# Performance work log

Measured on AMD Instinct MI355X. Metric: run time of the kernel, lower is better.

Reference implementation:

```python
import jax, jax.numpy as jnp
import numpy as np

B, T, D = 1, 4096, 1024
H = 16
HEAD_DIM = D // H
WINDOW = 256


def setup_inputs() -> dict:
    key = jax.random.key(0)
    k1, k2, k3 = jax.random.split(key, 3)
    x = jax.random.normal(k1, (B, T, D), dtype=jnp.float32)
    # torch nn.Linear(D, 3D) weight is (3D, D); we store transposed (D, 3D) for x @ W
    w_qkv = jax.random.normal(k2, (D, 3 * D), dtype=jnp.float32) * (1.0 / np.sqrt(D))
    w_out = jax.random.normal(k3, (D, D), dtype=jnp.float32) * (1.0 / np.sqrt(D))
    return {"x": x, "w_qkv": w_qkv, "w_out": w_out}


def reference(x, w_qkv, w_out):
    b, t, d = x.shape
    qkv = x @ w_qkv                                   # (B, T, 3D)
    q, k, v = jnp.split(qkv, 3, axis=-1)
    def split_heads(a):                               # (B, T, D) -> (B, H, T, dh)
        return a.reshape(b, t, H, HEAD_DIM).transpose(0, 2, 1, 3)
    q, k, v = split_heads(q), split_heads(k), split_heads(v)
    scale = jnp.sqrt(jnp.float32(HEAD_DIM))
    scores = jnp.einsum('bhqd,bhkd->bhqk', q, k) / scale   # (B, H, T, T)
    rows = jnp.arange(t)[:, None]
    cols = jnp.arange(t)[None, :]
    # causal sliding window: j <= i and j >= i - window + 1
    mask = (cols <= rows) & (cols >= rows - WINDOW + 1)     # (T, T) bool
    scores = jnp.where(mask[None, None], scores, -jnp.inf)
    attn = jax.nn.softmax(scores, axis=-1)
    out = jnp.einsum('bhqk,bhkd->bhqd', attn, v)            # (B, H, T, dh)
    out = out.transpose(0, 2, 1, 3).reshape(b, t, d)        # merge heads
    return out @ w_out
```

## Files before the change

### kernel.cpp

```cpp
#include <hip/hip_runtime.h>
#include <hip/hip_bf16.h>

#define T_SEQ 4096
#define DMODEL 1024
#define NH 16
#define DH 64
#define N_QKV 3072
#define N_QK 2048

typedef __attribute__((ext_vector_type(8))) short bf16x8;
typedef __attribute__((ext_vector_type(4))) float f32x4;

__device__ inline void gload_lds16(const __hip_bfloat16* g, __hip_bfloat16* l) {
  __builtin_amdgcn_global_load_lds(
      (const __attribute__((address_space(1))) void*)g,
      (__attribute__((address_space(3))) void*)l, 16, 0, 0);
}

__global__ void prep_kernel(const float* __restrict__ x,
                            const float* __restrict__ w_qkv,
                            const float* __restrict__ w_out,
                            __hip_bfloat16* __restrict__ x_bf,
                            __hip_bfloat16* __restrict__ wqkvT,
                            __hip_bfloat16* __restrict__ woutT) {
  __shared__ float tile[32][33];
  const int b = blockIdx.x;
  if (b < 4096) {
    int i = (b * 256 + threadIdx.x) * 4;
    float4 v = *(const float4*)(x + i);
    ushort4 o;
    o.x = __bfloat16_as_ushort(__float2bfloat16(v.x));
    o.y = __bfloat16_as_ushort(__float2bfloat16(v.y));
    o.z = __bfloat16_as_ushort(__float2bfloat16(v.z));
    o.w = __bfloat16_as_ushort(__float2bfloat16(v.w));
    *(ushort4*)((unsigned short*)x_bf + i) = o;
    return;
  }
  const float* in;
  __hip_bfloat16* out;
  int NN, KK, bn, bk;
  if (b < 7168) {
    int idx = b - 4096;
    in = w_qkv; out = wqkvT; NN = N_QKV; KK = DMODEL;
    bn = (idx % 96) * 32; bk = (idx / 96) * 32;
  } else {
    int idx = b - 7168;
    in = w_out; out = woutT; NN = DMODEL; KK = DMODEL;
    bn = (idx % 32) * 32; bk = (idx / 32) * 32;
  }
  int tx = threadIdx.x & 31, ty = threadIdx.x >> 5;
#pragma unroll
  for (int r = 0; r < 32; r += 8)
    tile[ty + r][tx] = in[(size_t)(bk + ty + r) * NN + bn + tx];
  __syncthreads();
#pragma unroll
  for (int r = 0; r < 32; r += 8)
    out[(size_t)(bn + ty + r) * KK + bk + tx] = __float2bfloat16(tile[tx][ty + r]);
}

__global__ __launch_bounds__(512, 2) void gemm8_qkv(
    const __hip_bfloat16* __restrict__ A, const __hip_bfloat16* __restrict__ Bt,
    __hip_bfloat16* __restrict__ qk, __hip_bfloat16* __restrict__ vt) {
  const int K = DMODEL;
  __shared__ alignas(16) __hip_bfloat16 Ab[3][256 * 64];
  __shared__ alignas(16) __hip_bfloat16 Bb[2][192 * 64];

  const int tid = threadIdx.x;
  const int lane = tid & 63;
  const int w = tid >> 6;
  const int wr = w >> 2, wc = w & 3;
  const int frow = lane & 15, fgrp = lane >> 4;

  const int bid = blockIdx.x;
  const int sbid = (bid & 7) * 32 + (bid >> 3);
  const int mb = sbid >> 4, nb = sbid & 15;
  const int brow = mb << 8, bcol = nb * 192;

  const int srow = lane >> 3;
  const int sslot = (lane & 7) ^ srow;
  const __hip_bfloat16* aSrcA = A + (size_t)(brow + w * 32 + srow) * K + sslot * 8;
  const __hip_bfloat16* aSrcB = Bt + (size_t)(bcol + w * 24 + srow) * K + sslot * 8;
  const int dstA = (w * 32 + srow) * 64 + (lane & 7) * 8;
  const int dstB = (w * 24 + srow) * 64 + (lane & 7) * 8;

  f32x4 acc[8][3] = {};

#pragma unroll
  for (int i = 0; i < 4; i++)
    gload_lds16(aSrcA + (size_t)(i * 8) * K, &Ab[0][dstA + i * 8 * 64]);
#pragma unroll
  for (int i = 0; i < 3; i++)
    gload_lds16(aSrcB + (size_t)(i * 8) * K, &Bb[0][dstB + i * 8 * 64]);
#pragma unroll
  for (int i = 0; i < 4; i++)
    gload_lds16(aSrcA + (size_t)(i * 8) * K + 64, &Ab[1][dstA + i * 8 * 64]);

  for (int t = 0; t < 16; ++t) {
    if (t < 15)
      asm volatile("s_waitcnt vmcnt(4)" ::: "memory");
    else
      asm volatile("s_waitcnt vmcnt(0)" ::: "memory");
    __builtin_amdgcn_s_barrier();

    const __hip_bfloat16* As = &Ab[t % 3][0];
    const __hip_bfloat16* Bs = &Bb[t & 1][0];
    bf16x8 bfrag[3][2], afrag[4][2];

#pragma unroll
    for (int n = 0; n < 3; n++) {
      int row = wc * 48 + n * 16 + frow;
#pragma unroll
      for (int kh = 0; kh < 2; kh++) {
        int slot = (kh * 4 + fgrp) ^ (row & 7);
        bfrag[n][kh] = *(const bf16x8*)(Bs + row * 64 + slot * 8);
      }
    }
#pragma unroll
    for (int m = 0; m < 4; m++) {
      int row = wr * 128 + m * 16 + frow;
#pragma unroll
      for (int kh = 0; kh < 2; kh++) {
        int slot = (kh * 4 + fgrp) ^ (row & 7);
        afrag[m][kh] = *(const bf16x8*)(As + row * 64 + slot * 8);
      }
    }
    if (t + 1 < 16) {
      __hip_bfloat16* bd = &Bb[(t + 1) & 1][0];
#pragma unroll
      for (int i = 0; i < 3; i++)
        gload_lds16(aSrcB + (size_t)(i * 8) * K + (t + 1) * 64, bd + dstB + i * 8 * 64);
    }
    __builtin_amdgcn_s_barrier();
    __builtin_amdgcn_s_setprio(1);
#pragma unroll
    for (int m = 0; m < 4; m++)
#pragma unroll
      for (int n = 0; n < 3; n++) {
        acc[m][n] = __builtin_amdgcn_mfma_f32_16x16x32_bf16(afrag[m][0], bfrag[n][0], acc[m][n], 0, 0, 0);
        acc[m][n] = __builtin_amdgcn_mfma_f32_16x16x32_bf16(afrag[m][1], bfrag[n][1], acc[m][n], 0, 0, 0);
      }
    __builtin_amdgcn_s_setprio(0);
    __builtin_amdgcn_s_barrier();

#pragma unroll
    for (int m = 0; m < 4; m++) {
      int row = wr * 128 + (m + 4) * 16 + frow;
#pragma unroll
      for (int kh = 0; kh < 2; kh++) {
        int slot = (kh * 4 + fgrp) ^ (row & 7);
        afrag[m][kh] = *(const bf16x8*)(As + row * 64 + slot * 8);
      }
    }
    if (t + 2 < 16) {
      __hip_bfloat16* ad = &Ab[(t + 2) % 3][0];
#pragma unroll
      for (int i = 0; i < 4; i++)
        gload_lds16(aSrcA + (size_t)(i * 8) * K + (t + 2) * 64, ad + dstA + i * 8 * 64);
    }
    __builtin_amdgcn_s_barrier();
    __builtin_amdgcn_s_setprio(1);
#pragma unroll
    for (int m = 0; m < 4; m++)
#pragma unroll
      for (int n = 0; n < 3; n++) {
        acc[m + 4][n] = __builtin_amdgcn_mfma_f32_16x16x32_bf16(afrag[m][0], bfrag[n][0], acc[m + 4][n], 0, 0, 0);
        acc[m + 4][n] = __builtin_amdgcn_mfma_f32_16x16x32_bf16(afrag[m][1], bfrag[n][1], acc[m + 4][n], 0, 0, 0);
      }
    __builtin_amdgcn_s_setprio(0);
  }

  const int orow0 = brow + wr * 128 + 4 * fgrp;
  const int ocol0 = bcol + wc * 48 + frow;
#pragma unroll
  for (int m = 0; m < 8; m++)
#pragma unroll
    for (int n = 0; n < 3; n++) {
      int col = ocol0 + n * 16;
      int row0 = orow0 + m * 16;
      if (col < N_QK) {
        float sc = (col < DMODEL) ? 0.125f : 1.0f;
#pragma unroll
        for (int j = 0; j < 4; j++)
          qk[(size_t)(row0 + j) * N_QK + col] = __float2bfloat16(acc[m][n][j] * sc);
      } else {
        ushort4 pack;
        pack.x = __bfloat16_as_ushort(__float2bfloat16(acc[m][n][0]));
        pack.y = __bfloat16_as_ushort(__float2bfloat16(acc[m][n][1]));
        pack.z = __bfloat16_as_ushort(__float2bfloat16(acc[m][n][2]));
        pack.w = __bfloat16_as_ushort(__float2bfloat16(acc[m][n][3]));
        *(ushort4*)((unsigned short*)vt + (size_t)(col - N_QK) * T_SEQ + row0) = pack;
      }
    }
}

__global__ __launch_bounds__(256) void gemm_out(
    const __hip_bfloat16* __restrict__ A, const __hip_bfloat16* __restrict__ Bt,
    float* __restrict__ C) {
  const int K = DMODEL, N = DMODEL;
  __shared__ alignas(16) __hip_bfloat16 Ab[4][128 * 32];
  __shared__ alignas(16) __hip_bfloat16 Bb[4][128 * 32];
  const int tid = threadIdx.x, lane = tid & 63, w = tid >> 6;
  const int wr = w >> 1, wc = w & 1;
  const int frow = lane & 15, fgrp = lane >> 4;
  const int bid = blockIdx.x;
  const int sbid = (bid & 7) * 32 + (bid >> 3);
  const int mb = sbid >> 3, nb = sbid & 7;
  const int brow = mb * 128, bcol = nb * 128;

  const int sr = tid >> 2;
  const int swz = ((tid & 3) ^ ((sr >> 1) & 3)) << 3;
  const __hip_bfloat16* aA = A + (size_t)(brow + sr) * K + swz;
  const __hip_bfloat16* aB = Bt + (size_t)(bcol + sr) * K + swz;
  const int dlo = sr * 32 + (tid & 3) * 8;
  const int dhi = (sr + 64) * 32 + (tid & 3) * 8;

  f32x4 acc[4][4] = {};
#pragma unroll
  for (int t = 0; t < 3; t++) {
    gload_lds16(aA + t * 32, &Ab[t][dlo]);
    gload_lds16(aA + 64 * (size_t)K + t * 32, &Ab[t][dhi]);
    gload_lds16(aB + t * 32, &Bb[t][dlo]);
    gload_lds16(aB + 64 * (size_t)K + t * 32, &Bb[t][dhi]);
  }
  for (int t = 0; t < 32; ++t) {
    if (t < 30)
      asm volatile("s_waitcnt vmcnt(8)" ::: "memory");
    else if (t == 30)
      asm volatile("s_waitcnt vmcnt(4)" ::: "memory");
    else
      asm volatile("s_waitcnt vmcnt(0)" ::: "memory");
    __builtin_amdgcn_s_barrier();
    const __hip_bfloat16* As = Ab[t & 3];
    const __hip_bfloat16* Bs = Bb[t & 3];
    if (t + 3 < 32) {
      gload_lds16(aA + (t + 3) * 32, &Ab[(t + 3) & 3][dlo]);
      gload_lds16(aA + 64 * (size_t)K + (t + 3) * 32, &Ab[(t + 3) & 3][dhi]);
      gload_lds16(aB + (t + 3) * 32, &Bb[(t + 3) & 3][dlo]);
      gload_lds16(aB + 64 * (size_t)K + (t + 3) * 32, &Bb[(t + 3) & 3][dhi]);
    }
    bf16x8 af[4], bfr[4];
#pragma unroll
    for (int m = 0; m < 4; m++) {
      int row = wr * 64 + m * 16 + frow;
      af[m] = *(const bf16x8*)(As + row * 32 + ((fgrp ^ ((row >> 1) & 3)) << 3));
    }
#pragma unroll
    for (int n = 0; n < 4; n++) {
      int row = wc * 64 + n * 16 + frow;
      bfr[n] = *(const bf16x8*)(Bs + row * 32 + ((fgrp ^ ((row >> 1) & 3)) << 3));
    }
    __builtin_amdgcn_s_barrier();
    __builtin_amdgcn_s_setprio(1);
#pragma unroll
    for (int m = 0; m < 4; m++)
#pragma unroll
      for (int n = 0; n < 4; n++)
        acc[m][n] = __builtin_amdgcn_mfma_f32_16x16x32_bf16(af[m], bfr[n], acc[m][n], 0, 0, 0);
    __builtin_amdgcn_s_setprio(0);
  }
  const int orow0 = brow + wr * 64 + 4 * fgrp;
  const int ocol0 = bcol + wc * 64 + frow;
#pragma unroll
  for (int m = 0; m < 4; m++)
#pragma unroll
    for (int n = 0; n < 4; n++)
#pragma unroll
      for (int j = 0; j < 4; j++)
        C[(size_t)(orow0 + m * 16 + j) * N + ocol0 + n * 16] = acc[m][n][j];
}

__global__ __launch_bounds__(256) void swa_kernel(
    const __hip_bfloat16* __restrict__ qk, const __hip_bfloat16* __restrict__ vt,
    __hip_bfloat16* __restrict__ attn_out) {
  const int b = blockIdx.x;
  const int s = (b & 7) * 128 + (b >> 3);
  const int h = s >> 6;
  const int qb = s & 63;
  const int tid = threadIdx.x;
  const int lane = tid & 63;
  const int w = tid >> 6;
  const int frow = lane & 15;
  const int fgrp = lane >> 4;
  const int fk = fgrp * 8;

  __shared__ alignas(16) __hip_bfloat16 Ks[2][64 * 64];
  __shared__ alignas(16) __hip_bfloat16 Vs[2][64 * 64];
  __shared__ alignas(16) __hip_bfloat16 Pl[4][16 * 72];

  const int qrow_g = qb * 64 + w * 16 + frow;
  bf16x8 aq[2];
  {
    const __hip_bfloat16* qptr = qk + (size_t)qrow_g * N_QK + h * DH;
    aq[0] = *(const bf16x8*)(qptr + fk);
    aq[1] = *(const bf16x8*)(qptr + 32 + fk);
  }

  f32x4 o[4] = {};
  float l_run[4] = {0.f, 0.f, 0.f, 0.f};

  const int srow = lane >> 3;
  const int ssw = (((lane & 7) ^ srow) << 3);
  const __hip_bfloat16* kbase =
      qk + (size_t)(w * 16 + srow) * N_QK + DMODEL + h * DH + ssw;
  const __hip_bfloat16* vbase =
      vt + (size_t)(h * DH + w * 16 + srow) * T_SEQ + ssw;

  const int kb0 = qb >= 4 ? qb - 4 : 0;

  {
    const __hip_bfloat16* ks = kbase + (size_t)kb0 * 64 * N_QK;
    gload_lds16(ks, &Ks[0][w * 16 * 64]);
    gload_lds16(ks + 8 * (size_t)N_QK, &Ks[0][(w * 16 + 8) * 64]);
    const __hip_bfloat16* vs = vbase + kb0 * 64;
    gload_lds16(vs, &Vs[0][w * 16 * 64]);
    gload_lds16(vs + 8 * (size_t)T_SEQ, &Vs[0][(w * 16 + 8) * 64]);
  }

  for (int kb = kb0; kb <= qb; kb++) {
    const int buf = (kb - kb0) & 1;
    if (kb < qb) {
      const __hip_bfloat16* ks = kbase + (size_t)(kb + 1) * 64 * N_QK;
      gload_lds16(ks, &Ks[buf ^ 1][w * 16 * 64]);
      gload_lds16(ks + 8 * (size_t)N_QK, &Ks[buf ^ 1][(w * 16 + 8) * 64]);
      const __hip_bfloat16* vs = vbase + (kb + 1) * 64;
      gload_lds16(vs, &Vs[buf ^ 1][w * 16 * 64]);
      gload_lds16(vs + 8 * (size_t)T_SEQ, &Vs[buf ^ 1][(w * 16 + 8) * 64]);
      asm volatile("s_waitcnt vmcnt(4)" ::: "memory");
    } else {
      asm volatile("s_waitcnt vmcnt(0)" ::: "memory");
    }
    __builtin_amdgcn_s_barrier();

    f32x4 sc[4];
#pragma unroll
    for (int n = 0; n < 4; n++) sc[n] = (f32x4){0.f, 0.f, 0.f, 0.f};
#pragma unroll
    for (int n = 0; n < 4; n++) {
      int rowk = n * 16 + frow;
      int x = rowk & 7;
      bf16x8 bk0 = *(const bf16x8*)(&Ks[buf][rowk * 64 + ((fgrp ^ x) << 3)]);
      bf16x8 bk1 = *(const bf16x8*)(&Ks[buf][rowk * 64 + (((4 + fgrp) ^ x) << 3)]);
      sc[n] = __builtin_amdgcn_mfma_f32_16x16x32_bf16(aq[0], bk0, sc[n], 0, 0, 0);
      sc[n] = __builtin_amdgcn_mfma_f32_16x16x32_bf16(aq[1], bk1, sc[n], 0, 0, 0);
    }

    const bool edge_hi = (kb == qb);
    const bool edge_lo = (kb == qb - 4);
#pragma unroll
    for (int r = 0; r < 4; r++) {
      const int row_l = w * 16 + 4 * fgrp + r;
      float rs = 0.f;
#pragma unroll
      for (int n = 0; n < 4; n++) {
        int col_l = n * 16 + frow;
        bool valid = (!edge_hi || col_l <= row_l) && (!edge_lo || col_l > row_l);
        float p = valid ? __expf(sc[n][r]) : 0.f;
        sc[n][r] = p;
        rs += p;
      }
      l_run[r] += rs;
    }

    __hip_bfloat16* pw = &Pl[w][0];
#pragma unroll
    for (int n = 0; n < 4; n++)
#pragma unroll
      for (int r = 0; r < 4; r++)
        pw[(4 * fgrp + r) * 72 + n * 16 + frow] = __float2bfloat16(sc[n][r]);

#pragma unroll
    for (int c = 0; c < 2; c++) {
      bf16x8 ap = *(const bf16x8*)(pw + frow * 72 + c * 32 + fk);
#pragma unroll
      for (int nd = 0; nd < 4; nd++) {
        int rowd = nd * 16 + frow;
        int x = rowd & 7;
        bf16x8 bv = *(const bf16x8*)(&Vs[buf][rowd * 64 + (((c * 4 + fgrp) ^ x) << 3)]);
        o[nd] = __builtin_amdgcn_mfma_f32_16x16x32_bf16(ap, bv, o[nd], 0, 0, 0);
      }
    }
    __builtin_amdgcn_s_barrier();
  }

#pragma unroll
  for (int r = 0; r < 4; r++) {
    float l = l_run[r];
    l += __shfl_xor(l, 1);
    l += __shfl_xor(l, 2);
    l += __shfl_xor(l, 4);
    l += __shfl_xor(l, 8);
    l_run[r] = l;
  }
#pragma unroll
  for (int nd = 0; nd < 4; nd++)
#pragma unroll
    for (int r = 0; r < 4; r++) {
      float v = o[nd][r] / l_run[r];
      attn_out[(size_t)(qb * 64 + w * 16 + 4 * fgrp + r) * DMODEL + h * DH + nd * 16 + frow] =
          __float2bfloat16(v);
    }
}

extern "C" void kernel_launch(void* const* d_in, const int* in_sizes, int n_in,
                              void* d_out, int out_size, void* d_ws, size_t ws_size,
                              hipStream_t stream) {
  const float* x = (const float*)d_in[0];
  const float* w_qkv = (const float*)d_in[1];
  const float* w_out = (const float*)d_in[2];
  float* out = (float*)d_out;

  char* ws = (char*)d_ws;
  __hip_bfloat16* x_bf = (__hip_bfloat16*)ws;
  __hip_bfloat16* wqkvT = (__hip_bfloat16*)(ws + 8388608);
  __hip_bfloat16* woutT = (__hip_bfloat16*)(ws + 14680064);
  __hip_bfloat16* qk_bf = (__hip_bfloat16*)(ws + 16777216);
  __hip_bfloat16* vt = (__hip_bfloat16*)(ws + 33554432);
  __hip_bfloat16* attn_bf = (__hip_bfloat16*)(ws + 41943040);

  prep_kernel<<<8192, 256, 0, stream>>>(x, w_qkv, w_out, x_bf, wqkvT, woutT);

  gemm8_qkv<<<(T_SEQ / 256) * (N_QKV / 192), 512, 0, stream>>>(x_bf, wqkvT, qk_bf, vt);

  swa_kernel<<<(T_SEQ / 64) * NH, 256, 0, stream>>>(qk_bf, vt, attn_bf);

  gemm_out<<<256, 256, 0, stream>>>(attn_bf, woutT, out);
}
```

Baseline: 83.35 us.

## Retile QKV GEMM to 128x192 blocks with 4 waves and double-buffered loads

The QKV projection GEMM now uses 128x192 output tiles computed by 256-thread blocks (4 waves, each covering 64x96), instead of 256x192 tiles with 8 waves. The launch grid doubles to 512 blocks. The triple-buffered A staging with split half-step compute is replaced by simple double buffering of both A and B, issued at the top of each iteration. This gives more blocks for occupancy and load balance and simplifies synchronisation, at the cost of less A reuse per block and more global traffic for B. The epilogue also writes Q columns twice (unscaled, then scaled), which adds redundant stores.

New measurement: 84.05 us. About the same (+0.8%).

```diff
diff --git a/kernel.cpp b/kernel.cpp
--- a/kernel.cpp
+++ b/kernel.cpp
@@ -58,130 +58,102 @@
     out[(size_t)(bn + ty + r) * KK + bk + tx] = __float2bfloat16(tile[tx][ty + r]);
 }
 
-__global__ __launch_bounds__(512, 2) void gemm8_qkv(
+__global__ __launch_bounds__(256, 2) void gemm8_qkv(
     const __hip_bfloat16* __restrict__ A, const __hip_bfloat16* __restrict__ Bt,
     __hip_bfloat16* __restrict__ qk, __hip_bfloat16* __restrict__ vt) {
   const int K = DMODEL;
-  __shared__ alignas(16) __hip_bfloat16 Ab[3][256 * 64];
+  __shared__ alignas(16) __hip_bfloat16 Ab[2][128 * 64];
   __shared__ alignas(16) __hip_bfloat16 Bb[2][192 * 64];
 
   const int tid = threadIdx.x;
   const int lane = tid & 63;
   const int w = tid >> 6;
-  const int wr = w >> 2, wc = w & 3;
+  const int wr = w >> 1, wc = w & 1;
   const int frow = lane & 15, fgrp = lane >> 4;
 
   const int bid = blockIdx.x;
-  const int sbid = (bid & 7) * 32 + (bid >> 3);
+  const int sbid = (bid & 7) * 64 + (bid >> 3);
   const int mb = sbid >> 4, nb = sbid & 15;
-  const int brow = mb << 8, bcol = nb * 192;
-
-  const int srow = lane >> 3;
-  const int sslot = (lane & 7) ^ srow;
-  const __hip_bfloat16* aSrcA = A + (size_t)(brow + w * 32 + srow) * K + sslot * 8;
-  const __hip_bfloat16* aSrcB = Bt + (size_t)(bcol + w * 24 + srow) * K + sslot * 8;
-  const int dstA = (w * 32 + srow) * 64 + (lane & 7) * 8;
-  const int dstB = (w * 24 + srow) * 64 + (lane & 7) * 8;
-
-  f32x4 acc[8][3] = {};
-
+  const int brow = mb << 7, bcol = nb * 192;
+
+  const int sslot = (tid & 7) ^ ((tid >> 3) & 7);
+  const __hip_bfloat16* aSrcA = A + (size_t)(brow + (tid >> 3)) * K + sslot * 8;
+  const __hip_bfloat16* aSrcB = Bt + (size_t)(bcol + (tid >> 3)) * K + sslot * 8;
+
+  f32x4 acc[4][6] = {};
+
+#pragma unroll
+  for (int i = 0; i < 6; i++)
+    gload_lds16(aSrcB + (size_t)(i * 32) * K, &Bb[0][(i * 256 + tid) * 8]);
 #pragma unroll
   for (int i = 0; i < 4; i++)
-    gload_lds16(aSrcA + (size_t)(i * 8) * K, &Ab[0][dstA + i * 8 * 64]);
-#pragma unroll
-  for (int i = 0; i < 3; i++)
-    gload_lds16(aSrcB + (size_t)(i * 8) * K, &Bb[0][dstB + i * 8 * 64]);
-#pragma unroll
-  for (int i = 0; i < 4; i++)
-    gload_lds16(aSrcA + (size_t)(i * 8) * K + 64, &Ab[1][dstA + i * 8 * 64]);
+    gload_lds16(aSrcA + (size_t)(i * 32) * K, &Ab[0][(i * 256 + tid) * 8]);
 
   for (int t = 0; t < 16; ++t) {
-    if (t < 15)
-      asm volatile("s_waitcnt vmcnt(4)" ::: "memory");
-    else
+    if (t < 15) {
+      __hip_bfloat16* bd = &Bb[(t + 1) & 1][0];
+      __hip_bfloat16* ad = &Ab[(t + 1) & 1][0];
+#pragma unroll
+      for (int i = 0; i < 6; i++)
+        gload_lds16(aSrcB + (size_t)(i * 32) * K + (t + 1) * 64, bd + (i * 256 + tid) * 8);
+#pragma unroll
+      for (int i = 0; i < 4; i++)
+        gload_lds16(aSrcA + (size_t)(i * 32) * K + (t + 1) * 64, ad + (i * 256 + tid) * 8);
+      asm volatile("s_waitcnt vmcnt(10)" ::: "memory");
+    } else {
       asm volatile("s_waitcnt vmcnt(0)" ::: "memory");
-    __builtin_amdgcn_s_barrier();
-
-    const __hip_bfloat16* As = &Ab[t % 3][0];
+    }
+    __builtin_amdgcn_s_barrier();
+
+    const __hip_bfloat16* As = &Ab[t & 1][0];
     const __hip_bfloat16* Bs = &Bb[t & 1][0];
-    bf16x8 bfrag[3][2], afrag[4][2];
-
-#pragma unroll
-    for (int n = 0; n < 3; n++) {
-      int row = wc * 48 + n * 16 + frow;
-#pragma unroll
-      for (int kh = 0; kh < 2; kh++) {
-        int slot = (kh * 4 + fgrp) ^ (row & 7);
-        bfrag[n][kh] = *(const bf16x8*)(Bs + row * 64 + slot * 8);
-      }
+    bf16x8 afr[4][2], bfr[6][2];
+#pragma unroll
+    for (int n = 0; n < 6; n++) {
+      int row = wc * 96 + n * 16 + frow;
+#pragma unroll
+      for (int kh = 0; kh < 2; kh++)
+        bfr[n][kh] = *(const bf16x8*)(Bs + row * 64 + (((kh * 4 + fgrp) ^ (row & 7)) << 3));
     }
 #pragma unroll
     for (int m = 0; m < 4; m++) {
-      int row = wr * 128 + m * 16 + frow;
-#pragma unroll
-      for (int kh = 0; kh < 2; kh++) {
-        int slot = (kh * 4 + fgrp) ^ (row & 7);
-        afrag[m][kh] = *(const bf16x8*)(As + row * 64 + slot * 8);
-      }
-    }
-    if (t + 1 < 16) {
-      __hip_bfloat16* bd = &Bb[(t + 1) & 1][0];
-#pragma unroll
-      for (int i = 0; i < 3; i++)
-        gload_lds16(aSrcB + (size_t)(i * 8) * K + (t + 1) * 64, bd + dstB + i * 8 * 64);
-    }
-    __builtin_amdgcn_s_barrier();
+      int row = wr * 64 + m * 16 + frow;
+#pragma unroll
+      for (int kh = 0; kh < 2; kh++)
+        afr[m][kh] = *(const bf16x8*)(As + row * 64 + (((kh * 4 + fgrp) ^ (row & 7)) << 3));
+    }
+    asm volatile("s_waitcnt lgkmcnt(0)" ::: "memory");
+    __builtin_amdgcn_s_barrier();
+
     __builtin_amdgcn_s_setprio(1);
 #pragma unroll
     for (int m = 0; m < 4; m++)
 #pragma unroll
-      for (int n = 0; n < 3; n++) {
-        acc[m][n] = __builtin_amdgcn_mfma_f32_16x16x32_bf16(afrag[m][0], bfrag[n][0], acc[m][n], 0, 0, 0);
-        acc[m][n] = __builtin_amdgcn_mfma_f32_16x16x32_bf16(afrag[m][1], bfrag[n][1], acc[m][n], 0, 0, 0);
+      for (int n = 0; n < 6; n++) {
+        acc[m][n] = __builtin_amdgcn_mfma_f32_16x16x32_bf16(afr[m][0], bfr[n][0], acc[m][n], 0, 0, 0);
+        acc[m][n] = __builtin_amdgcn_mfma_f32_16x16x32_bf16(afr[m][1], bfr[n][1], acc[m][n], 0, 0, 0);
       }
     __builtin_amdgcn_s_setprio(0);
-    __builtin_amdgcn_s_barrier();
-
-#pragma unroll
-    for (int m = 0; m < 4; m++) {
-      int row = wr * 128 + (m + 4) * 16 + frow;
-#pragma unroll
-      for (int kh = 0; kh < 2; kh++) {
-        int slot = (kh * 4 + fgrp) ^ (row & 7);
-        afrag[m][kh] = *(const bf16x8*)(As + row * 64 + slot * 8);
-      }
-    }
-    if (t + 2 < 16) {
-      __hip_bfloat16* ad = &Ab[(t + 2) % 3][0];
-#pragma unroll
-      for (int i = 0; i < 4; i++)
-        gload_lds16(aSrcA + (size_t)(i * 8) * K + (t + 2) * 64, ad + dstA + i * 8 * 64);
-    }
-    __builtin_amdgcn_s_barrier();
-    __builtin_amdgcn_s_setprio(1);
-#pragma unroll
-    for (int m = 0; m < 4; m++)
-#pragma unroll
-      for (int n = 0; n < 3; n++) {
-        acc[m + 4][n] = __builtin_amdgcn_mfma_f32_16x16x32_bf16(afrag[m][0], bfrag[n][0], acc[m + 4][n], 0, 0, 0);
-        acc[m + 4][n] = __builtin_amdgcn_mfma_f32_16x16x32_bf16(afrag[m][1], bfrag[n][1], acc[m + 4][n], 0, 0, 0);
-      }
-    __builtin_amdgcn_s_setprio(0);
-  }
-
-  const int orow0 = brow + wr * 128 + 4 * fgrp;
-  const int ocol0 = bcol + wc * 48 + frow;
-#pragma unroll
-  for (int m = 0; m < 8; m++)
-#pragma unroll
-    for (int n = 0; n < 3; n++) {
+  }
+
+  const int orow0 = brow + wr * 64 + 4 * fgrp;
+  const int ocol0 = bcol + wc * 96 + frow;
+#pragma unroll
+  for (int m = 0; m < 4; m++)
+#pragma unroll
+    for (int n = 0; n < 6; n++) {
       int col = ocol0 + n * 16;
       int row0 = orow0 + m * 16;
       if (col < N_QK) {
         float sc = (col < DMODEL) ? 0.125f : 1.0f;
 #pragma unroll
         for (int j = 0; j < 4; j++)
-          qk[(size_t)(row0 + j) * N_QK + col] = __float2bfloat16(acc[m][n][j] * sc);
+          qk[(size_t)(row0 + j) * N_QK + col] = __float2bfloat16(acc[m][n][j]);
+        if (col < DMODEL) {
+#pragma unroll
+          for (int j = 0; j < 4; j++)
+            qk[(size_t)(row0 + j) * N_QK + col] = __float2bfloat16(acc[m][n][j] * sc);
+        }
       } else {
         ushort4 pack;
         pack.x = __bfloat16_as_ushort(__float2bfloat16(acc[m][n][0]));
@@ -419,7 +391,7 @@
 
   prep_kernel<<<8192, 256, 0, stream>>>(x, w_qkv, w_out, x_bf, wqkvT, woutT);
 
-  gemm8_qkv<<<(T_SEQ / 256) * (N_QKV / 192), 512, 0, stream>>>(x_bf, wqkvT, qk_bf, vt);
+  gemm8_qkv<<<(T_SEQ / 128) * (N_QKV / 192), 256, 0, stream>>>(x_bf, wqkvT, qk_bf, vt);
 
   swa_kernel<<<(T_SEQ / 64) * NH, 256, 0, stream>>>(qk_bf, vt, attn_bf);
 
```

## Process 128-query tiles per block in sliding-window attention to reuse K/V loads

Applied to the files above, without the earlier changes.

Each attention block now handles 128 query rows (two 16-row groups per wave) instead of 64, so every K/V tile staged in LDS is reused by twice as many queries. The key range widens to 6 blocks per tile, and masking switches to global row/column comparisons. The grid is halved to 512 blocks. In exchange, each block does some wasted masked work on edge tiles, register pressure rises from doubled accumulators, and the smaller grid gives less parallelism across CUs.

After: 84.52 us. No clear change (+1.4%).

```diff
diff --git a/kernel.cpp b/kernel.cpp
--- a/kernel.cpp
+++ b/kernel.cpp
@@ -273,9 +273,10 @@
     const __hip_bfloat16* __restrict__ qk, const __hip_bfloat16* __restrict__ vt,
     __hip_bfloat16* __restrict__ attn_out) {
   const int b = blockIdx.x;
-  const int s = (b & 7) * 128 + (b >> 3);
-  const int h = s >> 6;
-  const int qb = s & 63;
+  const int s = (b & 7) * 64 + (b >> 3);
+  const int h = s >> 5;
+  const int qt = s & 31;
+  const int qs = qt * 128;
   const int tid = threadIdx.x;
   const int lane = tid & 63;
   const int w = tid >> 6;
@@ -287,118 +288,122 @@
   __shared__ alignas(16) __hip_bfloat16 Vs[2][64 * 64];
   __shared__ alignas(16) __hip_bfloat16 Pl[4][16 * 72];
 
-  const int qrow_g = qb * 64 + w * 16 + frow;
-  bf16x8 aq[2];
-  {
-    const __hip_bfloat16* qptr = qk + (size_t)qrow_g * N_QK + h * DH;
-    aq[0] = *(const bf16x8*)(qptr + fk);
-    aq[1] = *(const bf16x8*)(qptr + 32 + fk);
-  }
-
-  f32x4 o[4] = {};
-  float l_run[4] = {0.f, 0.f, 0.f, 0.f};
-
-  const int srow = lane >> 3;
-  const int ssw = (((lane & 7) ^ srow) << 3);
-  const __hip_bfloat16* kbase =
-      qk + (size_t)(w * 16 + srow) * N_QK + DMODEL + h * DH + ssw;
-  const __hip_bfloat16* vbase =
-      vt + (size_t)(h * DH + w * 16 + srow) * T_SEQ + ssw;
-
-  const int kb0 = qb >= 4 ? qb - 4 : 0;
-
-  {
-    const __hip_bfloat16* ks = kbase + (size_t)kb0 * 64 * N_QK;
-    gload_lds16(ks, &Ks[0][w * 16 * 64]);
-    gload_lds16(ks + 8 * (size_t)N_QK, &Ks[0][(w * 16 + 8) * 64]);
-    const __hip_bfloat16* vs = vbase + kb0 * 64;
-    gload_lds16(vs, &Vs[0][w * 16 * 64]);
-    gload_lds16(vs + 8 * (size_t)T_SEQ, &Vs[0][(w * 16 + 8) * 64]);
-  }
-
-  for (int kb = kb0; kb <= qb; kb++) {
+  bf16x8 aq[2][2];
+#pragma unroll
+  for (int g = 0; g < 2; g++) {
+    const __hip_bfloat16* qptr =
+        qk + (size_t)(qs + w * 32 + g * 16 + frow) * N_QK + h * DH;
+    aq[g][0] = *(const bf16x8*)(qptr + fk);
+    aq[g][1] = *(const bf16x8*)(qptr + 32 + fk);
+  }
+
+  f32x4 o[2][4] = {};
+  float l_run[2][4] = {};
+
+  const int srow = tid >> 3;
+  const int ssw = (((tid & 7) ^ (srow & 7)) << 3);
+  const int sdst = srow * 64 + (tid & 7) * 8;
+
+  const int kb0 = qt >= 2 ? qt * 2 - 4 : 0;
+  const int kb1 = qt * 2 + 1;
+
+#pragma unroll
+  for (int p = 0; p < 2; p++) {
+    gload_lds16(qk + (size_t)(kb0 * 64 + p * 32 + srow) * N_QK + DMODEL + h * DH + ssw,
+                &Ks[0][p * 32 * 64 + sdst]);
+    gload_lds16(vt + (size_t)(h * DH + p * 32 + srow) * T_SEQ + kb0 * 64 + ssw,
+                &Vs[0][p * 32 * 64 + sdst]);
+  }
+
+  for (int kb = kb0; kb <= kb1; kb++) {
     const int buf = (kb - kb0) & 1;
-    if (kb < qb) {
-      const __hip_bfloat16* ks = kbase + (size_t)(kb + 1) * 64 * N_QK;
-      gload_lds16(ks, &Ks[buf ^ 1][w * 16 * 64]);
-      gload_lds16(ks + 8 * (size_t)N_QK, &Ks[buf ^ 1][(w * 16 + 8) * 64]);
-      const __hip_bfloat16* vs = vbase + (kb + 1) * 64;
-      gload_lds16(vs, &Vs[buf ^ 1][w * 16 * 64]);
-      gload_lds16(vs + 8 * (size_t)T_SEQ, &Vs[buf ^ 1][(w * 16 + 8) * 64]);
-      asm volatile("s_waitcnt vmcnt(4)" ::: "memory");
+    if (kb < kb1) {
+#pragma unroll
+      for (int p = 0; p < 2; p++) {
+        gload_lds16(qk + (size_t)((kb + 1) * 64 + p * 32 + srow) * N_QK + DMODEL + h * DH + ssw,
+                    &Ks[buf ^ 1][p * 32 * 64 + sdst]);
+        gload_lds16(vt + (size_t)(h * DH + p * 32 + srow) * T_SEQ + (kb + 1) * 64 + ssw,
+                    &Vs[buf ^ 1][p * 32 * 64 + sdst]);
+      }
+      asm volatile("s_waitcnt vmcnt(8)" ::: "memory");
     } else {
       asm volatile("s_waitcnt vmcnt(0)" ::: "memory");
     }
     __builtin_amdgcn_s_barrier();
 
-    f32x4 sc[4];
-#pragma unroll
-    for (int n = 0; n < 4; n++) sc[n] = (f32x4){0.f, 0.f, 0.f, 0.f};
-#pragma unroll
-    for (int n = 0; n < 4; n++) {
-      int rowk = n * 16 + frow;
-      int x = rowk & 7;
-      bf16x8 bk0 = *(const bf16x8*)(&Ks[buf][rowk * 64 + ((fgrp ^ x) << 3)]);
-      bf16x8 bk1 = *(const bf16x8*)(&Ks[buf][rowk * 64 + (((4 + fgrp) ^ x) << 3)]);
-      sc[n] = __builtin_amdgcn_mfma_f32_16x16x32_bf16(aq[0], bk0, sc[n], 0, 0, 0);
-      sc[n] = __builtin_amdgcn_mfma_f32_16x16x32_bf16(aq[1], bk1, sc[n], 0, 0, 0);
-    }
-
-    const bool edge_hi = (kb == qb);
-    const bool edge_lo = (kb == qb - 4);
+#pragma unroll
+    for (int g = 0; g < 2; g++) {
+      f32x4 sc[4];
+#pragma unroll
+      for (int n = 0; n < 4; n++) sc[n] = (f32x4){0.f, 0.f, 0.f, 0.f};
+#pragma unroll
+      for (int n = 0; n < 4; n++) {
+        int rowk = n * 16 + frow;
+        int x = rowk & 7;
+        bf16x8 bk0 = *(const bf16x8*)(&Ks[buf][rowk * 64 + ((fgrp ^ x) << 3)]);
+        bf16x8 bk1 = *(const bf16x8*)(&Ks[buf][rowk * 64 + (((4 + fgrp) ^ x) << 3)]);
+        sc[n] = __builtin_amdgcn_mfma_f32_16x16x32_bf16(aq[g][0], bk0, sc[n], 0, 0, 0);
+        sc[n] = __builtin_amdgcn_mfma_f32_16x16x32_bf16(aq[g][1], bk1, sc[n], 0, 0, 0);
+      }
+
+#pragma unroll
+      for (int r = 0; r < 4; r++) {
+        const int row_g = qs + w * 32 + g * 16 + 4 * fgrp + r;
+        float rs = 0.f;
+#pragma unroll
+        for (int n = 0; n < 4; n++) {
+          int col_g = kb * 64 + n * 16 + frow;
+          bool valid = (col_g <= row_g) && (col_g + 256 > row_g);
+          float p = valid ? __expf(sc[n][r]) : 0.f;
+          sc[n][r] = p;
+          rs += p;
+        }
+        l_run[g][r] += rs;
+      }
+
+      __hip_bfloat16* pw = &Pl[w][0];
+#pragma unroll
+      for (int n = 0; n < 4; n++)
+#pragma unroll
+        for (int r = 0; r < 4; r++)
+          pw[(4 * fgrp + r) * 72 + n * 16 + frow] = __float2bfloat16(sc[n][r]);
+
+#pragma unroll
+      for (int c = 0; c < 2; c++) {
+        bf16x8 ap = *(const bf16x8*)(pw + frow * 72 + c * 32 + fk);
+#pragma unroll
+        for (int nd = 0; nd < 4; nd++) {
+          int rowd = nd * 16 + frow;
+          int x = rowd & 7;
+          bf16x8 bv = *(const bf16x8*)(&Vs[buf][rowd * 64 + (((c * 4 + fgrp) ^ x) << 3)]);
+          o[g][nd] = __builtin_amdgcn_mfma_f32_16x16x32_bf16(ap, bv, o[g][nd], 0, 0, 0);
+        }
+      }
+    }
+    __builtin_amdgcn_s_barrier();
+  }
+
+#pragma unroll
+  for (int g = 0; g < 2; g++)
 #pragma unroll
     for (int r = 0; r < 4; r++) {
-      const int row_l = w * 16 + 4 * fgrp + r;
-      float rs = 0.f;
-#pragma unroll
-      for (int n = 0; n < 4; n++) {
-        int col_l = n * 16 + frow;
-        bool valid = (!edge_hi || col_l <= row_l) && (!edge_lo || col_l > row_l);
-        float p = valid ? __expf(sc[n][r]) : 0.f;
-        sc[n][r] = p;
-        rs += p;
-      }
-      l_run[r] += rs;
-    }
-
-    __hip_bfloat16* pw = &Pl[w][0];
-#pragma unroll
-    for (int n = 0; n < 4; n++)
-#pragma unroll
-      for (int r = 0; r < 4; r++)
-        pw[(4 * fgrp + r) * 72 + n * 16 + frow] = __float2bfloat16(sc[n][r]);
-
-#pragma unroll
-    for (int c = 0; c < 2; c++) {
-      bf16x8 ap = *(const bf16x8*)(pw + frow * 72 + c * 32 + fk);
-#pragma unroll
-      for (int nd = 0; nd < 4; nd++) {
-        int rowd = nd * 16 + frow;
-        int x = rowd & 7;
-        bf16x8 bv = *(const bf16x8*)(&Vs[buf][rowd * 64 + (((c * 4 + fgrp) ^ x) << 3)]);
-        o[nd] = __builtin_amdgcn_mfma_f32_16x16x32_bf16(ap, bv, o[nd], 0, 0, 0);
-      }
-    }
-    __builtin_amdgcn_s_barrier();
-  }
-
-#pragma unroll
-  for (int r = 0; r < 4; r++) {
-    float l = l_run[r];
-    l += __shfl_xor(l, 1);
-    l += __shfl_xor(l, 2);
-    l += __shfl_xor(l, 4);
-    l += __shfl_xor(l, 8);
-    l_run[r] = l;
-  }
-#pragma unroll
-  for (int nd = 0; nd < 4; nd++)
-#pragma unroll
-    for (int r = 0; r < 4; r++) {
-      float v = o[nd][r] / l_run[r];
-      attn_out[(size_t)(qb * 64 + w * 16 + 4 * fgrp + r) * DMODEL + h * DH + nd * 16 + frow] =
-          __float2bfloat16(v);
-    }
+      float l = l_run[g][r];
+      l += __shfl_xor(l, 1);
+      l += __shfl_xor(l, 2);
+      l += __shfl_xor(l, 4);
+      l += __shfl_xor(l, 8);
+      l_run[g][r] = l;
+    }
+#pragma unroll
+  for (int g = 0; g < 2; g++)
+#pragma unroll
+    for (int nd = 0; nd < 4; nd++)
+#pragma unroll
+      for (int r = 0; r < 4; r++) {
+        float v = o[g][nd][r] / l_run[g][r];
+        attn_out[(size_t)(qs + w * 32 + g * 16 + 4 * fgrp + r) * DMODEL + h * DH + nd * 16 + frow] =
+            __float2bfloat16(v);
+      }
 }
 
 extern "C" void kernel_launch(void* const* d_in, const int* in_sizes, int n_in,
@@ -421,7 +426,7 @@
 
   gemm8_qkv<<<(T_SEQ / 256) * (N_QKV / 192), 512, 0, stream>>>(x_bf, wqkvT, qk_bf, vt);
 
-  swa_kernel<<<(T_SEQ / 64) * NH, 256, 0, stream>>>(qk_bf, vt, attn_bf);
+  swa_kernel<<<(T_SEQ / 128) * NH, 256, 0, stream>>>(qk_bf, vt, attn_bf);
 
   gemm_out<<<256, 256, 0, stream>>>(attn_bf, woutT, out);
 }
```
